# Performance work log

Hardware: AMD Instinct MI355X
Metric: run time of the kernel (lower is better)

## Reference

```python
import jax, jax.numpy as jnp
import numpy as np


def setup_inputs() -> dict:
    key = jax.random.key(0)
    k1, k2, k3 = jax.random.split(key, 3)
    N, H = 16384, 4096
    x = jax.random.normal(k1, (N, H), dtype=jnp.float32)
    weight = jax.random.normal(k2, (H,), dtype=jnp.float32)
    bias = jax.random.normal(k3, (H,), dtype=jnp.float32)
    return {"x": x, "weight": weight, "bias": bias}


def reference(x, weight, bias):
    # F.linear(x, diag(weight), bias) == x * weight + bias (per-feature scale+shift)
    return x * weight + bias
```

## Files before the change

### kernel.cpp

```cpp
#include <hip/hip_runtime.h>
#include <hip/hip_bf16.h>


__global__ __launch_bounds__(256) void scale_shift_f32(
    const float4* __restrict__ x,
    const float4* __restrict__ w,
    const float4* __restrict__ b,
    float4* __restrict__ out,
    int total4, int h4mask) {
    int stride = gridDim.x * blockDim.x;
    for (int i = blockIdx.x * blockDim.x + threadIdx.x; i < total4; i += stride) {
        int h4 = i & h4mask;
        float4 xv = x[i];
        float4 wv = w[h4];
        float4 bv = b[h4];
        float4 o;
        o.x = fmaf(xv.x, wv.x, bv.x);
        o.y = fmaf(xv.y, wv.y, bv.y);
        o.z = fmaf(xv.z, wv.z, bv.z);
        o.w = fmaf(xv.w, wv.w, bv.w);
        out[i] = o;
    }
}

extern "C" void kernel_launch(void* const* d_in, const int* in_sizes, int n_in,
                              void* d_out, int out_size, void* d_ws, size_t ws_size,
                              hipStream_t stream) {
    const float* x = (const float*)d_in[0];
    const float* w = (const float*)d_in[1];
    const float* b = (const float*)d_in[2];
    float* out = (float*)d_out;

    const int H = in_sizes[1];
    const int total = out_size;
    const int total4 = total / 4;
    const int h4mask = H / 4 - 1;

    const int block = 256;
    int grid = (total4 + block - 1) / block;
    if (grid > 2048) grid = 2048;

    scale_shift_f32<<<grid, block, 0, stream>>>(
        (const float4*)x, (const float4*)w, (const float4*)b,
        (float4*)out, total4, h4mask);
}
```

Measured before the change: 107.3 us.

## Hoist weight/bias loads, unroll by four, use nontemporal loads and stores

Picks a grid whose stride is a multiple of H/4, so each thread's feature index stays fixed and weight and bias are loaded once per thread instead of every iteration. The main loop is unrolled four ways to put more loads in flight, and x and out go through nontemporal loads and stores to avoid polluting the cache on a pure streaming op. This relies on H/4 dividing grid*block. The wrong-result risk is mitigated by the grid search loop, but the grid can shrink if H is unusual.

```diff
diff --git a/kernel.cpp b/kernel.cpp
--- a/kernel.cpp
+++ b/kernel.cpp
@@ -2,24 +2,42 @@
 #include <hip/hip_bf16.h>
 
 
-__global__ __launch_bounds__(256) void scale_shift_f32(
-    const float4* __restrict__ x,
-    const float4* __restrict__ w,
-    const float4* __restrict__ b,
-    float4* __restrict__ out,
+typedef float v4f __attribute__((ext_vector_type(4)));
+
+__global__ __launch_bounds__(256) void scale_shift_f32_hoist(
+    const v4f* __restrict__ x,
+    const v4f* __restrict__ w,
+    const v4f* __restrict__ b,
+    v4f* __restrict__ out,
     int total4, int h4mask) {
-    int stride = gridDim.x * blockDim.x;
-    for (int i = blockIdx.x * blockDim.x + threadIdx.x; i < total4; i += stride) {
-        int h4 = i & h4mask;
-        float4 xv = x[i];
-        float4 wv = w[h4];
-        float4 bv = b[h4];
-        float4 o;
-        o.x = fmaf(xv.x, wv.x, bv.x);
-        o.y = fmaf(xv.y, wv.y, bv.y);
-        o.z = fmaf(xv.z, wv.z, bv.z);
-        o.w = fmaf(xv.w, wv.w, bv.w);
-        out[i] = o;
+    const int tid = blockIdx.x * blockDim.x + threadIdx.x;
+    const int stride = gridDim.x * blockDim.x;
+
+    const int h4 = tid & h4mask;
+    const v4f wv = w[h4];
+    const v4f bv = b[h4];
+
+    int i = tid;
+    for (; i + 3 * stride < total4; i += 4 * stride) {
+        v4f x0 = __builtin_nontemporal_load(&x[i]);
+        v4f x1 = __builtin_nontemporal_load(&x[i + stride]);
+        v4f x2 = __builtin_nontemporal_load(&x[i + 2 * stride]);
+        v4f x3 = __builtin_nontemporal_load(&x[i + 3 * stride]);
+
+        v4f o0 = x0 * wv + bv;
+        v4f o1 = x1 * wv + bv;
+        v4f o2 = x2 * wv + bv;
+        v4f o3 = x3 * wv + bv;
+
+        __builtin_nontemporal_store(o0, &out[i]);
+        __builtin_nontemporal_store(o1, &out[i + stride]);
+        __builtin_nontemporal_store(o2, &out[i + 2 * stride]);
+        __builtin_nontemporal_store(o3, &out[i + 3 * stride]);
+    }
+    for (; i < total4; i += stride) {
+        v4f xv = __builtin_nontemporal_load(&x[i]);
+        v4f o = xv * wv + bv;
+        __builtin_nontemporal_store(o, &out[i]);
     }
 }
 
@@ -34,13 +52,14 @@
     const int H = in_sizes[1];
     const int total = out_size;
     const int total4 = total / 4;
-    const int h4mask = H / 4 - 1;
+    const int h4 = H / 4;
+    const int h4mask = h4 - 1;
 
     const int block = 256;
-    int grid = (total4 + block - 1) / block;
-    if (grid > 2048) grid = 2048;
+    int grid = 2048;
+    while ((long long)grid * block % h4 != 0 && grid > 1) grid--;
 
-    scale_shift_f32<<<grid, block, 0, stream>>>(
-        (const float4*)x, (const float4*)w, (const float4*)b,
-        (float4*)out, total4, h4mask);
+    scale_shift_f32_hoist<<<grid, block, 0, stream>>>(
+        (const v4f*)x, (const v4f*)w, (const v4f*)b,
+        (v4f*)out, total4, h4mask);
 }
```

New measurement: 126.8 us. 1.18x slower.
